# Kernel optimization log

Hardware: AMD Instinct MI355X
Metric: run time of the kernel (lower is better)

Reference implementation:

```python
import jax, jax.numpy as jnp
import numpy as np
from jax import lax

# Grid / layer constants matching init_kwargs
D, H, W = 41, 159, 159   # spatial_shape (chosen so (dim-K) % S == 0)
K = 3                    # kernel_size
S = 2                    # stride
CIN, COUT = 32, 64       # in_channels, out_channels
B = 2                    # batch_size
N_PER_BATCH = 75000      # active voxels per batch element (unique coords)


def setup_inputs() -> dict:
    # Unique active-voxel coordinates per batch (spconv assumes no duplicates).
    rng = np.random.default_rng(0)
    nvox = D * H * W
    rows = []
    for b in range(B):
        lin = rng.choice(nvox, size=N_PER_BATCH, replace=False)
        z = lin // (H * W)
        y = (lin // W) % H
        x = lin % W
        rows.append(np.stack([np.full(N_PER_BATCH, b), z, y, x], axis=1))
    coors = jnp.asarray(np.concatenate(rows, axis=0), dtype=jnp.int32)  # [N,4]

    key = jax.random.key(0)
    k1, k2, k3 = jax.random.split(key, 3)
    features = jax.random.normal(k1, (B * N_PER_BATCH, CIN), dtype=jnp.float32)
    # SparseConv3d weight (no bias): kernel [K,K,K,CIN,COUT] in DHWIO layout.
    w1 = (jax.random.normal(k2, (K, K, K, CIN, COUT), dtype=jnp.float32) * 0.05)
    # SparseInverseConv3d weight: transpose-conv mapping COUT -> CIN; stored in
    # forward-conv DHWIO layout [K,K,K,CIN,COUT] and applied via conv_transpose
    # with transpose_kernel=True (the exact adjoint of the forward conv op).
    w2 = (jax.random.normal(k3, (K, K, K, CIN, COUT), dtype=jnp.float32) * 0.05)
    return {"features": features, "coors": coors, "batch_size": B, "w1": w1, "w2": w2}


def reference(features, coors, batch_size, w1, w2):
    # Scatter active features into a dense NDHWC grid (equivalent to the sparse
    # tensor; SparseConv3d with bias=False gives identical values on active sites).
    b, z, y, x = coors[:, 0], coors[:, 1], coors[:, 2], coors[:, 3]
    dense = jnp.zeros((batch_size, D, H, W, CIN), features.dtype).at[b, z, y, x].set(features)
    # Mask of originally-active sites: SparseInverseConv3d (shared indice_key)
    # only produces outputs at these sites, and ToDense zeros everything else.
    mask = jnp.zeros((batch_size, D, H, W, 1), features.dtype).at[b, z, y, x].set(1.0)

    dn = ("NDHWC", "DHWIO", "NDHWC")
    # SparseConv3d(CIN->COUT, k=3, s=2): strided VALID conv.
    mid = lax.conv_general_dilated(dense, w1, (S, S, S), "VALID", dimension_numbers=dn)
    # SparseInverseConv3d(COUT->CIN): exact transpose of the forward conv's
    # gather/scatter pattern; recovers the original spatial shape.
    back = lax.conv_transpose(mid, w2, (S, S, S), "VALID", dimension_numbers=dn,
                              transpose_kernel=True)
    out = back * mask  # restrict to original active sites, zeros elsewhere
    return jnp.transpose(out, (0, 4, 1, 2, 3))  # ToDense returns NCDHW
```

## Files before the change

### kernel.cpp

```cpp
#include <hip/hip_runtime.h>

#define D_   41
#define H_   159
#define W_   159
#define MD   20
#define MH   79
#define MW   79
#define CIN  32
#define COUT 64
#define BATCH 2

#define NTAP 27
#define WLDS (NTAP * 16 * 64)

#define BLK   1024
#define WPB   (BLK / 64)

typedef unsigned int u32;

static __device__ __forceinline__ u32 bf16_rn(float x) {
    u32 u = __float_as_uint(x);
    return (u + 0x7fffu + ((u >> 16) & 1u)) >> 16;
}
static __device__ __forceinline__ float bf_lo(u32 p) { return __uint_as_float(p << 16); }
static __device__ __forceinline__ float bf_hi(u32 p) { return __uint_as_float(p & 0xffff0000u); }

__global__ void pack_kernel(const float* __restrict__ w1, const float* __restrict__ w2,
                            u32* __restrict__ w1p, u32* __restrict__ w2p) {
    int i = blockIdx.x * 256 + threadIdx.x;
    if (i >= WLDS) return;
    int k  = i & 3;
    int co = (i >> 2) & 63;
    int j4 = (i >> 8) & 3;
    int t  = i >> 10;
    int j  = j4 * 4 + k;
    int s0 = (t * 32 + 2 * j) * 64 + co;
    int s1 = (t * 32 + 2 * j + 1) * 64 + co;
    w1p[i] = bf16_rn(w1[s0]) | (bf16_rn(w1[s1]) << 16);
    w2p[i] = bf16_rn(w2[s0]) | (bf16_rn(w2[s1]) << 16);
}

__global__ void scatter_idx_kernel(const int* __restrict__ coors,
                                   int* __restrict__ idx, int n) {
    int i = blockIdx.x * blockDim.x + threadIdx.x;
    if (i >= n) return;
    int4 c = ((const int4*)coors)[i];
    idx[((c.x * D_ + c.y) * H_ + c.z) * W_ + c.w] = i;
}

#define LOADW(dst, t)                                              \
    {                                                              \
        const uint4* wq = (const uint4*)lw + (t) * 256 + lane;     \
        uint4 q0 = wq[0], q1 = wq[64], q2 = wq[128], q3 = wq[192]; \
        dst[0] = q0.x;  dst[1] = q0.y;  dst[2] = q0.z;  dst[3] = q0.w;   \
        dst[4] = q1.x;  dst[5] = q1.y;  dst[6] = q1.z;  dst[7] = q1.w;   \
        dst[8] = q2.x;  dst[9] = q2.y;  dst[10] = q2.z; dst[11] = q2.w;  \
        dst[12] = q3.x; dst[13] = q3.y; dst[14] = q3.z; dst[15] = q3.w;  \
    }

__global__ __launch_bounds__(BLK) void mid_kernel(const float* __restrict__ feat,
                                                  const int* __restrict__ idx,
                                                  const u32* __restrict__ w1p,
                                                  float* __restrict__ mid) {
    __shared__ u32 lw[WLDS];
    for (int i = threadIdx.x; i < WLDS; i += BLK) lw[i] = w1p[i];
    __syncthreads();

    const int NV = BATCH * MD * MH * MW;
    int lane = threadIdx.x & 63;
    int wid  = threadIdx.x >> 6;
    int nw   = gridDim.x * WPB;
    int gw   = blockIdx.x * WPB + wid;
    int per  = (NV + nw - 1) / nw;
    int v0   = gw * per;
    int v1   = v0 + per; if (v1 > NV) v1 = NV;

    int l  = lane < NTAP ? lane : NTAP - 1;
    int kz = l / 9, kr = l % 9, ky = kr / 3, kx = kr % 3;

    auto probe = [&](int v) -> int {
        if (v >= v1 || lane >= NTAP) return -1;
        int xo = v % MW; int t0 = v / MW;
        int yo = t0 % MH; t0 /= MH;
        int zo = t0 % MD; int b = t0 / MD;
        return idx[((b * D_ + 2 * zo + kz) * H_ + 2 * yo + ky) * W_ + 2 * xo + kx];
    };

    int pA = probe(v0), pB = probe(v0 + 1);
    for (int v = v0; v < v1; v += 2) {
        int cA = pA, cB = pB;
        pA = probe(v + 2);
        pB = probe(v + 3);
        unsigned long long mA = __ballot(cA >= 0);
        unsigned long long mB = __ballot(cB >= 0);

        float a0 = 0.f, a1 = 0.f, b0 = 0.f, b1 = 0.f;
        while (mA | mB) {
            bool hA = mA != 0, hB = mB != 0;
            float4 fav[8], fbv[8];
            u32 wav[16], wbv[16];
            if (hA) {
                int t = (int)__builtin_ctzll(mA); mA &= mA - 1;
                int pp = __shfl(cA, t);
                const float4* f4 = (const float4*)(feat + (size_t)pp * CIN);
                #pragma unroll
                for (int q = 0; q < 8; ++q) fav[q] = f4[q];
                LOADW(wav, t)
            }
            if (hB) {
                int t = (int)__builtin_ctzll(mB); mB &= mB - 1;
                int pp = __shfl(cB, t);
                const float4* f4 = (const float4*)(feat + (size_t)pp * CIN);
                #pragma unroll
                for (int q = 0; q < 8; ++q) fbv[q] = f4[q];
                LOADW(wbv, t)
            }
            if (hA) {
                #pragma unroll
                for (int q = 0; q < 8; ++q) {
                    a0 = fmaf(fav[q].x, bf_lo(wav[2 * q + 0]), a0);
                    a1 = fmaf(fav[q].y, bf_hi(wav[2 * q + 0]), a1);
                    a0 = fmaf(fav[q].z, bf_lo(wav[2 * q + 1]), a0);
                    a1 = fmaf(fav[q].w, bf_hi(wav[2 * q + 1]), a1);
                }
            }
            if (hB) {
                #pragma unroll
                for (int q = 0; q < 8; ++q) {
                    b0 = fmaf(fbv[q].x, bf_lo(wbv[2 * q + 0]), b0);
                    b1 = fmaf(fbv[q].y, bf_hi(wbv[2 * q + 0]), b1);
                    b0 = fmaf(fbv[q].z, bf_lo(wbv[2 * q + 1]), b0);
                    b1 = fmaf(fbv[q].w, bf_hi(wbv[2 * q + 1]), b1);
                }
            }
        }
        mid[(size_t)v * COUT + lane] = a0 + a1;
        if (v + 1 < v1) mid[(size_t)(v + 1) * COUT + lane] = b0 + b1;
    }
}

#define BSTEP(MK, HALF)                                            \
    {                                                              \
        bool up = (lane & MK) != 0;                                \
        _Pragma("unroll")                                          \
        for (int k = 0; k < HALF; ++k) {                           \
            float send = up ? acc[k] : acc[k + HALF];              \
            float keep = up ? acc[k + HALF] : acc[k];              \
            acc[k] = keep + __shfl_xor(send, MK, 64);              \
        }                                                          \
    }

__global__ __launch_bounds__(BLK) void out_kernel(const int* __restrict__ coors,
                                                  const float* __restrict__ mid,
                                                  const u32* __restrict__ w2p,
                                                  float* __restrict__ compact, int n) {
    __shared__ u32 lw[WLDS];
    for (int i = threadIdx.x; i < WLDS; i += BLK) lw[i] = w2p[i];
    __syncthreads();

    int lane = threadIdx.x & 63;
    int wid  = threadIdx.x >> 6;
    int nw   = gridDim.x * WPB;
    int gw   = blockIdx.x * WPB + wid;
    int per  = (n + nw - 1) / nw;
    int i0   = gw * per;
    int i1   = i0 + per; if (i1 > n) i1 = n;

    int l  = lane < NTAP ? lane : NTAP - 1;
    int kz = l / 9, kr = l % 9, ky = kr / 3, kx = kr % 3;

    const int4* cvec = (const int4*)coors;
    int4 nc = make_int4(0, 0, 0, 0);
    if (i0 < i1) nc = cvec[i0];

    for (int i = i0; i < i1; ++i) {
        int4 c = nc;
        if (i + 1 < i1) nc = cvec[i + 1];
        int b = c.x, z = c.y, y = c.z, x = c.w;

        int zr = z - kz, yr = y - ky, xr = x - kx;
        bool ok = (lane < NTAP) &&
                  zr >= 0 && !(zr & 1) && (zr >> 1) < MD &&
                  yr >= 0 && !(yr & 1) && (yr >> 1) < MH &&
                  xr >= 0 && !(xr & 1) && (xr >> 1) < MW;
        int vv = ok ? ((b * MD + (zr >> 1)) * MH + (yr >> 1)) * MW + (xr >> 1) : -1;
        unsigned long long m = __ballot(ok);

        float acc[CIN];
        #pragma unroll
        for (int ci = 0; ci < CIN; ++ci) acc[ci] = 0.f;

        while (m) {
            int t0 = (int)__builtin_ctzll(m); m &= m - 1;
            bool h1 = (m != 0);
            int t1 = 0;
            if (h1) { t1 = (int)__builtin_ctzll(m); m &= m - 1; }

            int ve0 = __shfl(vv, t0);
            float mr0 = mid[(size_t)ve0 * COUT + lane];
            u32 wv0[16];
            LOADW(wv0, t0)

            float mr1 = 0.f; u32 wv1[16];
            if (h1) {
                int ve1 = __shfl(vv, t1);
                mr1 = mid[(size_t)ve1 * COUT + lane];
                LOADW(wv1, t1)
            }

            #pragma unroll
            for (int j = 0; j < 16; ++j) {
                acc[2 * j + 0] = fmaf(mr0, bf_lo(wv0[j]), acc[2 * j + 0]);
                acc[2 * j + 1] = fmaf(mr0, bf_hi(wv0[j]), acc[2 * j + 1]);
            }
            if (h1) {
                #pragma unroll
                for (int j = 0; j < 16; ++j) {
                    acc[2 * j + 0] = fmaf(mr1, bf_lo(wv1[j]), acc[2 * j + 0]);
                    acc[2 * j + 1] = fmaf(mr1, bf_hi(wv1[j]), acc[2 * j + 1]);
                }
            }
        }

        BSTEP(32, 16)
        BSTEP(16, 8)
        BSTEP(8, 4)
        BSTEP(4, 2)
        BSTEP(2, 1)
        float s = acc[0] + __shfl_xor(acc[0], 1, 64);
        if (!(lane & 1))
            compact[(size_t)i * CIN + (lane >> 1)] = s;
    }
}

__global__ __launch_bounds__(256) void expand_kernel(const int* __restrict__ idx,
                                                     const float* __restrict__ compact,
                                                     float* __restrict__ out) {
    const int HW    = H_ * W_;
    const int PLANE = D_ * HW;
    const int NVOX  = BATCH * PLANE;
    int g = blockIdx.x * 256 + threadIdx.x;
    if (g >= NVOX) return;

    int p   = idx[g];
    int b   = g / PLANE;
    int rem = g - b * PLANE;

    float r[CIN];
    if (p >= 0) {
        const float4* row = (const float4*)(compact + (size_t)p * CIN);
        #pragma unroll
        for (int q = 0; q < 8; ++q) {
            float4 v = row[q];
            r[4 * q + 0] = v.x; r[4 * q + 1] = v.y;
            r[4 * q + 2] = v.z; r[4 * q + 3] = v.w;
        }
    } else {
        #pragma unroll
        for (int q = 0; q < CIN; ++q) r[q] = 0.f;
    }

    float* o = out + (size_t)b * ((size_t)CIN * PLANE) + rem;
    #pragma unroll
    for (int ci = 0; ci < CIN; ++ci)
        __builtin_nontemporal_store(r[ci], o + (size_t)ci * PLANE);
}

extern "C" void kernel_launch(void* const* d_in, const int* in_sizes, int n_in,
                              void* d_out, int out_size, void* d_ws, size_t ws_size,
                              hipStream_t stream) {
    const float* feat  = (const float*)d_in[0];
    const int*   coors = (const int*)d_in[1];
    const float* w1    = (const float*)d_in[3];
    const float* w2    = (const float*)d_in[4];
    float*       out   = (float*)d_out;

    int n = in_sizes[0] / CIN;

    int*   idx      = (int*)d_ws;
    size_t idxBytes = (size_t)BATCH * D_ * H_ * W_ * sizeof(int);
    size_t midOff   = (idxBytes + 255) & ~(size_t)255;
    float* mid      = (float*)((char*)d_ws + midOff);
    size_t wOff     = midOff + (size_t)BATCH * MD * MH * MW * COUT * sizeof(float);
    wOff            = (wOff + 255) & ~(size_t)255;
    u32*   w1p      = (u32*)((char*)d_ws + wOff);
    u32*   w2p      = w1p + WLDS;
    float* compact  = (float*)(w2p + WLDS);

    (void)hipMemsetAsync(idx, 0xFF, idxBytes, stream);

    pack_kernel<<<(WLDS + 255) / 256, 256, 0, stream>>>(w1, w2, w1p, w2p);
    scatter_idx_kernel<<<(n + 255) / 256, 256, 0, stream>>>(coors, idx, n);

    mid_kernel<<<256, BLK, 0, stream>>>(feat, idx, w1p, mid);
    out_kernel<<<256, BLK, 0, stream>>>(coors, mid, w2p, compact, n);

    const int NVOX = BATCH * D_ * H_ * W_;
    expand_kernel<<<(NVOX + 255) / 256, 256, 0, stream>>>(idx, compact, out);
}
```

Baseline: 621.5 us.

## Split mid conv output channels across block pairs with half-size weight LDS

The mid kernel now assigns each block to one half of the output channels, so the shared-memory weight copy is halved. Within a wave, two lanes share one output channel and each covers half of the input channels, then the partial sums are combined with a shuffle. The grid doubles to 512 blocks so both halves cover every voxel. This cuts per-lane register use for weights and features and lowers LDS footprint, which may raise occupancy. In exchange, every voxel's idx probes and feature gathers are repeated by two blocks, and half the lanes sit idle during the store.

```diff
diff --git a/kernel.cpp b/kernel.cpp
--- a/kernel.cpp
+++ b/kernel.cpp
@@ -11,7 +11,8 @@
 #define BATCH 2
 
 #define NTAP 27
-#define WLDS (NTAP * 16 * 64)
+#define WLDS  (NTAP * 16 * 64)
+#define WLDS1H (NTAP * 512)
 
 #define BLK   1024
 #define WPB   (BLK / 64)
@@ -29,15 +30,31 @@
                             u32* __restrict__ w1p, u32* __restrict__ w2p) {
     int i = blockIdx.x * 256 + threadIdx.x;
     if (i >= WLDS) return;
-    int k  = i & 3;
-    int co = (i >> 2) & 63;
-    int j4 = (i >> 8) & 3;
-    int t  = i >> 10;
-    int j  = j4 * 4 + k;
-    int s0 = (t * 32 + 2 * j) * 64 + co;
-    int s1 = (t * 32 + 2 * j + 1) * 64 + co;
-    w1p[i] = bf16_rn(w1[s0]) | (bf16_rn(w1[s1]) << 16);
-    w2p[i] = bf16_rn(w2[s0]) | (bf16_rn(w2[s1]) << 16);
+    {
+        int k  = i & 3;
+        int co = (i >> 2) & 63;
+        int j4 = (i >> 8) & 3;
+        int t  = i >> 10;
+        int j  = j4 * 4 + k;
+        int s0 = (t * 32 + 2 * j) * 64 + co;
+        int s1 = (t * 32 + 2 * j + 1) * 64 + co;
+        w2p[i] = bf16_rn(w2[s0]) | (bf16_rn(w2[s1]) << 16);
+    }
+    {
+        int h    = i / WLDS1H;
+        int r    = i - h * WLDS1H;
+        int k    = r & 3;
+        int co_l = (r >> 2) & 31;
+        int j4   = (r >> 7) & 1;
+        int q    = (r >> 8) & 1;
+        int t    = r >> 9;
+        int jl   = j4 * 4 + k;
+        int ci   = q * 16 + 2 * jl;
+        int co   = h * 32 + co_l;
+        int s0 = (t * 32 + ci) * 64 + co;
+        int s1 = (t * 32 + ci + 1) * 64 + co;
+        w1p[i] = bf16_rn(w1[s0]) | (bf16_rn(w1[s1]) << 16);
+    }
 }
 
 __global__ void scatter_idx_kernel(const int* __restrict__ coors,
@@ -62,18 +79,22 @@
                                                   const int* __restrict__ idx,
                                                   const u32* __restrict__ w1p,
                                                   float* __restrict__ mid) {
-    __shared__ u32 lw[WLDS];
-    for (int i = threadIdx.x; i < WLDS; i += BLK) lw[i] = w1p[i];
+    __shared__ u32 lw[WLDS1H];
+    int H = blockIdx.x & 1;
+    for (int i = threadIdx.x; i < WLDS1H; i += BLK) lw[i] = w1p[H * WLDS1H + i];
     __syncthreads();
 
     const int NV = BATCH * MD * MH * MW;
     int lane = threadIdx.x & 63;
     int wid  = threadIdx.x >> 6;
-    int nw   = gridDim.x * WPB;
-    int gw   = blockIdx.x * WPB + wid;
+    int nw   = (gridDim.x >> 1) * WPB;
+    int gw   = (blockIdx.x >> 1) * WPB + wid;
     int per  = (NV + nw - 1) / nw;
     int v0   = gw * per;
     int v1   = v0 + per; if (v1 > NV) v1 = NV;
+
+    int co_l = lane >> 1;
+    int q    = lane & 1;
 
     int l  = lane < NTAP ? lane : NTAP - 1;
     int kz = l / 9, kr = l % 9, ky = kr / 3, kx = kr % 3;
@@ -97,45 +118,53 @@
         float a0 = 0.f, a1 = 0.f, b0 = 0.f, b1 = 0.f;
         while (mA | mB) {
             bool hA = mA != 0, hB = mB != 0;
-            float4 fav[8], fbv[8];
-            u32 wav[16], wbv[16];
+            float4 fa0, fa1, fa2, fa3, fb0, fb1, fb2, fb3;
+            uint4 wa0, wa1, wb0, wb1;
             if (hA) {
                 int t = (int)__builtin_ctzll(mA); mA &= mA - 1;
                 int pp = __shfl(cA, t);
-                const float4* f4 = (const float4*)(feat + (size_t)pp * CIN);
-                #pragma unroll
-                for (int q = 0; q < 8; ++q) fav[q] = f4[q];
-                LOADW(wav, t)
+                const float4* f4 = (const float4*)(feat + (size_t)pp * CIN) + q * 4;
+                fa0 = f4[0]; fa1 = f4[1]; fa2 = f4[2]; fa3 = f4[3];
+                const uint4* wq = (const uint4*)lw + (t * 4 + q * 2) * 32 + co_l;
+                wa0 = wq[0]; wa1 = wq[32];
             }
             if (hB) {
                 int t = (int)__builtin_ctzll(mB); mB &= mB - 1;
                 int pp = __shfl(cB, t);
-                const float4* f4 = (const float4*)(feat + (size_t)pp * CIN);
-                #pragma unroll
-                for (int q = 0; q < 8; ++q) fbv[q] = f4[q];
-                LOADW(wbv, t)
+                const float4* f4 = (const float4*)(feat + (size_t)pp * CIN) + q * 4;
+                fb0 = f4[0]; fb1 = f4[1]; fb2 = f4[2]; fb3 = f4[3];
+                const uint4* wq = (const uint4*)lw + (t * 4 + q * 2) * 32 + co_l;
+                wb0 = wq[0]; wb1 = wq[32];
             }
             if (hA) {
-                #pragma unroll
-                for (int q = 0; q < 8; ++q) {
-                    a0 = fmaf(fav[q].x, bf_lo(wav[2 * q + 0]), a0);
-                    a1 = fmaf(fav[q].y, bf_hi(wav[2 * q + 0]), a1);
-                    a0 = fmaf(fav[q].z, bf_lo(wav[2 * q + 1]), a0);
-                    a1 = fmaf(fav[q].w, bf_hi(wav[2 * q + 1]), a1);
-                }
+                a0 = fmaf(fa0.x, bf_lo(wa0.x), a0);  a1 = fmaf(fa0.y, bf_hi(wa0.x), a1);
+                a0 = fmaf(fa0.z, bf_lo(wa0.y), a0);  a1 = fmaf(fa0.w, bf_hi(wa0.y), a1);
+                a0 = fmaf(fa1.x, bf_lo(wa0.z), a0);  a1 = fmaf(fa1.y, bf_hi(wa0.z), a1);
+                a0 = fmaf(fa1.z, bf_lo(wa0.w), a0);  a1 = fmaf(fa1.w, bf_hi(wa0.w), a1);
+                a0 = fmaf(fa2.x, bf_lo(wa1.x), a0);  a1 = fmaf(fa2.y, bf_hi(wa1.x), a1);
+                a0 = fmaf(fa2.z, bf_lo(wa1.y), a0);  a1 = fmaf(fa2.w, bf_hi(wa1.y), a1);
+                a0 = fmaf(fa3.x, bf_lo(wa1.z), a0);  a1 = fmaf(fa3.y, bf_hi(wa1.z), a1);
+                a0 = fmaf(fa3.z, bf_lo(wa1.w), a0);  a1 = fmaf(fa3.w, bf_hi(wa1.w), a1);
             }
             if (hB) {
-                #pragma unroll
-                for (int q = 0; q < 8; ++q) {
-                    b0 = fmaf(fbv[q].x, bf_lo(wbv[2 * q + 0]), b0);
-                    b1 = fmaf(fbv[q].y, bf_hi(wbv[2 * q + 0]), b1);
-                    b0 = fmaf(fbv[q].z, bf_lo(wbv[2 * q + 1]), b0);
-                    b1 = fmaf(fbv[q].w, bf_hi(wbv[2 * q + 1]), b1);
-                }
+                b0 = fmaf(fb0.x, bf_lo(wb0.x), b0);  b1 = fmaf(fb0.y, bf_hi(wb0.x), b1);
+                b0 = fmaf(fb0.z, bf_lo(wb0.y), b0);  b1 = fmaf(fb0.w, bf_hi(wb0.y), b1);
+                b0 = fmaf(fb1.x, bf_lo(wb0.z), b0);  b1 = fmaf(fb1.y, bf_hi(wb0.z), b1);
+                b0 = fmaf(fb1.z, bf_lo(wb0.w), b0);  b1 = fmaf(fb1.w, bf_hi(wb0.w), b1);
+                b0 = fmaf(fb2.x, bf_lo(wb1.x), b0);  b1 = fmaf(fb2.y, bf_hi(wb1.x), b1);
+                b0 = fmaf(fb2.z, bf_lo(wb1.y), b0);  b1 = fmaf(fb2.w, bf_hi(wb1.y), b1);
+                b0 = fmaf(fb3.x, bf_lo(wb1.z), b0);  b1 = fmaf(fb3.y, bf_hi(wb1.z), b1);
+                b0 = fmaf(fb3.z, bf_lo(wb1.w), b0);  b1 = fmaf(fb3.w, bf_hi(wb1.w), b1);
             }
         }
-        mid[(size_t)v * COUT + lane] = a0 + a1;
-        if (v + 1 < v1) mid[(size_t)(v + 1) * COUT + lane] = b0 + b1;
+        float sA = a0 + a1;
+        sA += __shfl_xor(sA, 1, 64);
+        float sB = b0 + b1;
+        sB += __shfl_xor(sB, 1, 64);
+        if (q == 0) {
+            mid[(size_t)v * COUT + H * 32 + co_l] = sA;
+            if (v + 1 < v1) mid[(size_t)(v + 1) * COUT + H * 32 + co_l] = sB;
+        }
     }
 }
 
@@ -292,7 +321,7 @@
     pack_kernel<<<(WLDS + 255) / 256, 256, 0, stream>>>(w1, w2, w1p, w2p);
     scatter_idx_kernel<<<(n + 255) / 256, 256, 0, stream>>>(coors, idx, n);
 
-    mid_kernel<<<256, BLK, 0, stream>>>(feat, idx, w1p, mid);
+    mid_kernel<<<512, BLK, 0, stream>>>(feat, idx, w1p, mid);
     out_kernel<<<256, BLK, 0, stream>>>(coors, mid, w2p, compact, n);
 
     const int NVOX = BATCH * D_ * H_ * W_;
```

After: 674.8 us. 8.6% more time.

## Reorder features into spatial order via count/prefix/place before mid conv

Applied to the files above, without the earlier changes.

Adds a count, prefix-sum and place pass that copies active features into a spatially ordered compact array and builds a matching index grid, so the mid kernel's feature gathers hit nearby memory. It also remaps block IDs in the mid kernel to spread spatial ranges across XCDs/L2 slices. This costs three extra kernel launches and extra passes over the full dense index grid plus a feature copy. The within-block atomic counter keeps ordering only approximately spatial.

```diff
diff --git a/kernel.cpp b/kernel.cpp
--- a/kernel.cpp
+++ b/kernel.cpp
@@ -15,6 +15,9 @@
 
 #define BLK   1024
 #define WPB   (BLK / 64)
+
+#define SGRID 256
+#define SBLK  256
 
 typedef unsigned int u32;
 
@@ -48,6 +51,66 @@
     idx[((c.x * D_ + c.y) * H_ + c.z) * W_ + c.w] = i;
 }
 
+
+__global__ __launch_bounds__(SBLK) void count_kernel(const int* __restrict__ idx,
+                                                     int* __restrict__ counts) {
+    const int NG = BATCH * D_ * H_ * W_;
+    int per = (NG + SGRID - 1) / SGRID;
+    int g0 = blockIdx.x * per;
+    int g1 = g0 + per; if (g1 > NG) g1 = NG;
+    int c = 0;
+    for (int g = g0 + threadIdx.x; g < g1; g += SBLK) c += (idx[g] >= 0);
+    __shared__ int sc[SBLK];
+    sc[threadIdx.x] = c;
+    __syncthreads();
+    for (int s = SBLK / 2; s > 0; s >>= 1) {
+        if (threadIdx.x < s) sc[threadIdx.x] += sc[threadIdx.x + s];
+        __syncthreads();
+    }
+    if (threadIdx.x == 0) counts[blockIdx.x] = sc[0];
+}
+
+__global__ __launch_bounds__(SGRID) void prefix_kernel(int* __restrict__ counts,
+                                                       int* __restrict__ bases) {
+    __shared__ int tmp[SGRID];
+    int t = threadIdx.x;
+    tmp[t] = counts[t];
+    __syncthreads();
+    for (int off = 1; off < SGRID; off <<= 1) {
+        int u = (t >= off) ? tmp[t - off] : 0;
+        __syncthreads();
+        tmp[t] += u;
+        __syncthreads();
+    }
+    bases[t] = (t == 0) ? 0 : tmp[t - 1];
+}
+
+__global__ __launch_bounds__(SBLK) void place_kernel(const int* __restrict__ idx,
+                                                     const float* __restrict__ feat,
+                                                     const int* __restrict__ bases,
+                                                     float* __restrict__ feat_s,
+                                                     int* __restrict__ idxs) {
+    const int NG = BATCH * D_ * H_ * W_;
+    int per = (NG + SGRID - 1) / SGRID;
+    int g0 = blockIdx.x * per;
+    int g1 = g0 + per; if (g1 > NG) g1 = NG;
+    __shared__ int ctr;
+    if (threadIdx.x == 0) ctr = bases[blockIdx.x];
+    __syncthreads();
+    for (int g = g0 + threadIdx.x; g < g1; g += SBLK) {
+        int p = idx[g];
+        int r = -1;
+        if (p >= 0) {
+            r = atomicAdd(&ctr, 1);
+            const float4* s = (const float4*)(feat + (size_t)p * CIN);
+            float4* d = (float4*)(feat_s + (size_t)r * CIN);
+            #pragma unroll
+            for (int q = 0; q < 8; ++q) d[q] = s[q];
+        }
+        idxs[g] = r;
+    }
+}
+
 #define LOADW(dst, t)                                              \
     {                                                              \
         const uint4* wq = (const uint4*)lw + (t) * 256 + lane;     \
@@ -58,19 +121,21 @@
         dst[12] = q3.x; dst[13] = q3.y; dst[14] = q3.z; dst[15] = q3.w;  \
     }
 
-__global__ __launch_bounds__(BLK) void mid_kernel(const float* __restrict__ feat,
-                                                  const int* __restrict__ idx,
+__global__ __launch_bounds__(BLK) void mid_kernel(const float* __restrict__ feat_s,
+                                                  const int* __restrict__ idxs,
                                                   const u32* __restrict__ w1p,
                                                   float* __restrict__ mid) {
     __shared__ u32 lw[WLDS];
     for (int i = threadIdx.x; i < WLDS; i += BLK) lw[i] = w1p[i];
     __syncthreads();
 
+    int sb = (blockIdx.x & 7) * 32 + (blockIdx.x >> 3);
+
     const int NV = BATCH * MD * MH * MW;
     int lane = threadIdx.x & 63;
     int wid  = threadIdx.x >> 6;
     int nw   = gridDim.x * WPB;
-    int gw   = blockIdx.x * WPB + wid;
+    int gw   = sb * WPB + wid;
     int per  = (NV + nw - 1) / nw;
     int v0   = gw * per;
     int v1   = v0 + per; if (v1 > NV) v1 = NV;
@@ -83,7 +148,7 @@
         int xo = v % MW; int t0 = v / MW;
         int yo = t0 % MH; t0 /= MH;
         int zo = t0 % MD; int b = t0 / MD;
-        return idx[((b * D_ + 2 * zo + kz) * H_ + 2 * yo + ky) * W_ + 2 * xo + kx];
+        return idxs[((b * D_ + 2 * zo + kz) * H_ + 2 * yo + ky) * W_ + 2 * xo + kx];
     };
 
     int pA = probe(v0), pB = probe(v0 + 1);
@@ -102,7 +167,7 @@
             if (hA) {
                 int t = (int)__builtin_ctzll(mA); mA &= mA - 1;
                 int pp = __shfl(cA, t);
-                const float4* f4 = (const float4*)(feat + (size_t)pp * CIN);
+                const float4* f4 = (const float4*)(feat_s + (size_t)pp * CIN);
                 #pragma unroll
                 for (int q = 0; q < 8; ++q) fav[q] = f4[q];
                 LOADW(wav, t)
@@ -110,7 +175,7 @@
             if (hB) {
                 int t = (int)__builtin_ctzll(mB); mB &= mB - 1;
                 int pp = __shfl(cB, t);
-                const float4* f4 = (const float4*)(feat + (size_t)pp * CIN);
+                const float4* f4 = (const float4*)(feat_s + (size_t)pp * CIN);
                 #pragma unroll
                 for (int q = 0; q < 8; ++q) fbv[q] = f4[q];
                 LOADW(wbv, t)
@@ -286,13 +351,21 @@
     u32*   w1p      = (u32*)((char*)d_ws + wOff);
     u32*   w2p      = w1p + WLDS;
     float* compact  = (float*)(w2p + WLDS);
+    float* feat_s   = compact + (size_t)n * CIN;
+    int*   idxs     = (int*)(feat_s + (size_t)n * CIN);
+    int*   counts   = idxs + (size_t)BATCH * D_ * H_ * W_;
+    int*   bases    = counts + SGRID;
 
     (void)hipMemsetAsync(idx, 0xFF, idxBytes, stream);
 
     pack_kernel<<<(WLDS + 255) / 256, 256, 0, stream>>>(w1, w2, w1p, w2p);
     scatter_idx_kernel<<<(n + 255) / 256, 256, 0, stream>>>(coors, idx, n);
 
-    mid_kernel<<<256, BLK, 0, stream>>>(feat, idx, w1p, mid);
+    count_kernel<<<SGRID, SBLK, 0, stream>>>(idx, counts);
+    prefix_kernel<<<1, SGRID, 0, stream>>>(counts, bases);
+    place_kernel<<<SGRID, SBLK, 0, stream>>>(idx, feat, bases, feat_s, idxs);
+
+    mid_kernel<<<256, BLK, 0, stream>>>(feat_s, idxs, w1p, mid);
     out_kernel<<<256, BLK, 0, stream>>>(coors, mid, w2p, compact, n);
 
     const int NVOX = BATCH * D_ * H_ * W_;
```

After: 657.9 us. +5.9%, slower.
